# Performance work log

Measured on AMD Instinct MI355X. Metric: run time of the kernel, lower is better.

## Reference

```python
import jax, jax.numpy as jnp
import numpy as np
from jax import lax


def T_grid(t, num_coeff):
    # Chebyshev polynomials T_0..T_{N-1} evaluated at t -> (N, len(t))
    rows = [jnp.ones_like(t), t]
    for _ in range(2, num_coeff):
        rows.append(2.0 * t * rows[-1] - rows[-2])
    return jnp.stack(rows[:num_coeff], axis=0)


def setup_inputs() -> dict:
    key = jax.random.key(0)
    k1, k2, k3, k4, k5 = jax.random.split(key, 5)
    B, D, H, N, T = 128, 512, 1024, 32, 16
    return {
        "t_span": jnp.linspace(0.0, 1.0, T, dtype=jnp.float32),
        "y_init": jax.random.normal(k1, (B, D), dtype=jnp.float32),
        "B_init": jax.random.uniform(k2, (B, D, N), dtype=jnp.float32),
        "W1": jax.random.normal(k3, (D, H), dtype=jnp.float32) / jnp.sqrt(jnp.float32(D)),
        "b1": jax.random.normal(k4, (H,), dtype=jnp.float32),
        "W2": jax.random.normal(k5, (H, D), dtype=jnp.float32) / jnp.sqrt(jnp.float32(H)),
        "num_coeff_per_dim": 32,
        "max_iters": 10,
    }


def reference(t_span, y_init, B_init, W1, b1, W2, num_coeff_per_dim, max_iters):
    N = num_coeff_per_dim
    t0, t1 = t_span[0], t_span[-1]

    # Chebyshev-Gauss-Lobatto nodes on [-1, 1] and Simpson midpoints interleaved
    t_cheb = -jnp.cos(jnp.pi * (jnp.arange(N, dtype=t_span.dtype) / (N - 1)))  # (N,)
    mids = 0.5 * (t_cheb[1:] + t_cheb[:-1])
    t_simpsons = jnp.zeros(2 * N - 1, dtype=t_span.dtype).at[::2].set(t_cheb).at[1::2].set(mids)
    t_true = t0 + 0.5 * (t1 - t0) * (t_simpsons + 1.0)  # (2N-1,)

    Phi_f = T_grid(t_simpsons, N)        # (N, 2N-1)
    Phi = Phi_f[:, ::2]                  # (N, N), invert ONCE (reused every iter)
    Phi_inv = jnp.linalg.inv(Phi)
    widths = (t_true[2::2] - t_true[:-2:2]) / 6.0  # (N-1,) Simpson interval weights

    def f_all(Y):  # vector field f(t, y) = tanh(y @ W1 + t*b1) @ W2, all nodes at once
        # Y: (B, D, M) with M = 2N-1
        h = jnp.tanh(jnp.einsum("bdm,dh->bhm", Y, W1) + t_true[None, None, :] * b1[None, :, None])
        return jnp.einsum("bhm,hd->bdm", h, W2)

    def step(Bc, _):
        approx = jnp.einsum("bdn,nm->bdm", Bc, Phi_f)          # (B, D, 2N-1)
        fap = f_all(approx)
        # Simpson's rule per Chebyshev interval, then cumulative integral S
        s = widths * (fap[..., :-2:2] + 4.0 * fap[..., 1:-1:2] + fap[..., 2::2])  # (B,D,N-1)
        S = jnp.concatenate([jnp.zeros_like(s[..., :1]), jnp.cumsum(s, axis=-1)], axis=-1)
        # torch.linalg.solve(Phi, S + y0, left=False): Bn @ Phi = S + y0
        Bn = (S + y_init[..., None]) @ Phi_inv
        return Bn, None

    B_final, _ = lax.scan(step, B_init, None, length=max_iters)

    t_out = -1.0 + 2.0 * (t_span - t0) / (t1 - t0)
    Phi_out = T_grid(t_out, N)                                  # (N, T)
    approx = jnp.einsum("bdn,nt->bdt", B_final, Phi_out)        # (B, D, T)
    return jnp.moveaxis(approx, -1, 0), B_final                 # (T, B, D), (B, D, N)
```

## Files before the change

kernel.cpp:

```cpp
#include <hip/hip_runtime.h>
#include <hip/hip_bf16.h>
#include <math.h>

#define BB 128
#define DD 512
#define HH 1024
#define NB 32
#define MM 63
#define TT 16
#define ITERS 10

#define OFF_U       0
#define OFF_TTRUE   64
#define OFF_PHIOUT  128
#define OFF_PHIF_BF 1024
#define OFF_QT_BF   2048
#define HDRF        4096
#define OFF_PTPA    HDRF
#define OFF_PTP0    (OFF_PTPA + 2097152)
#define OFF_W1P     (OFF_PTP0 + 2097152)
#define OFF_W2P     (OFF_W1P + 262144)
#define OFF_WWP     (OFF_W2P + 262144)
#define OFF_YW1     (OFF_WWP + 524288)

typedef __attribute__((ext_vector_type(8))) short bf16x8;
typedef __attribute__((ext_vector_type(4))) float f32x4;

static __device__ __forceinline__ unsigned short f2bf(float f) {
    unsigned int x = __builtin_bit_cast(unsigned int, f);
    unsigned int r = x + 0x7FFFu + ((x >> 16) & 1u);
    return (unsigned short)(r >> 16);
}

static __device__ __forceinline__ void store4bf(unsigned short* p,
                                                float v0, float v1, float v2, float v3) {
    unsigned int lo = (unsigned int)f2bf(v0) | ((unsigned int)f2bf(v1) << 16);
    unsigned int hi = (unsigned int)f2bf(v2) | ((unsigned int)f2bf(v3) << 16);
    uint2 u; u.x = lo; u.y = hi;
    *(uint2*)p = u;
}

static __device__ __forceinline__ float tanh_fast(float x) {
    float e = exp2f(x * 2.88539008177793f);
    return 1.0f - 2.0f / (e + 1.0f);
}

static __device__ __forceinline__ unsigned short* aS(unsigned short* smA, int r, int c16) {
    return (unsigned short*)((char*)smA + (((r << 10) + (c16 << 4)) ^ ((r & 7) << 4)));
}

__global__ __launch_bounds__(256) void prologue_kernel(
        const float* __restrict__ t_span, const float* __restrict__ W1,
        const float* __restrict__ W2, const float* __restrict__ y_init,
        float* __restrict__ ws) {
    __shared__ __align__(16) char smem[66560];
    const int bid  = blockIdx.x;
    const int t    = threadIdx.x;
    const int lane = t & 63;
    const int w    = t >> 6;
    const int q    = lane >> 4;
    const int l15  = lane & 15;

    if (bid == 0) {
        double* tsim    = (double*)(smem + 0);
        double* ttrue_d = (double*)(smem + 512);
        double* wid     = (double*)(smem + 1024);
        double* phid    = (double*)(smem + 1280);
        double* pinv    = (double*)(smem + 17408);
        double* Rl      = (double*)(smem + 34048);
        double* Qd      = (double*)(smem + 50176);

        const double PI = 3.14159265358979323846;
        const double t0 = (double)t_span[0];
        const double t1 = (double)t_span[TT - 1];

        if (t < MM) {
            double v;
            if ((t & 1) == 0) {
                int j = t >> 1;
                v = -cos(PI * (double)j / (double)(NB - 1));
            } else {
                int i = t >> 1;
                double a = -cos(PI * (double)i / (double)(NB - 1));
                double b = -cos(PI * (double)(i + 1) / (double)(NB - 1));
                v = 0.5 * (a + b);
            }
            tsim[t] = v;
            ttrue_d[t] = t0 + 0.5 * (t1 - t0) * (v + 1.0);
        }
        __syncthreads();
        if (t < 31) wid[t] = (ttrue_d[2 * t + 2] - ttrue_d[2 * t]) / 6.0;
        if (t < MM) ws[OFF_TTRUE + t] = (float)ttrue_d[t];
        if (t == 63) ws[OFF_TTRUE + 63] = 0.0f;

        if (t < MM) {
            double x = tsim[t];
            double r0 = 1.0, r1 = x;
            phid[0 * MM + t] = r0;
            phid[1 * MM + t] = r1;
            for (int n = 2; n < NB; n++) {
                double r2 = 2.0 * x * r1 - r0;
                phid[n * MM + t] = r2;
                r0 = r1; r1 = r2;
            }
        }

        for (int f = t; f < NB * NB; f += 256) {
            int i = f >> 5, j = f & 31;
            double ci = (i == 0 || i == NB - 1) ? 2.0 : 1.0;
            double cj = (j == 0 || j == NB - 1) ? 2.0 : 1.0;
            double v = 2.0 * cos(PI * (double)(i * j) / (double)(NB - 1))
                       / ((double)(NB - 1) * ci * cj);
            pinv[f] = (j & 1) ? -v : v;
        }
        __syncthreads();

        {
            unsigned short* pf = (unsigned short*)(ws + OFF_PHIF_BF);
            for (int f = t; f < 64 * 32; f += 256) {
                int m = f >> 5, n = f & 31;
                pf[f] = f2bf(m < MM ? (float)phid[n * MM + m] : 0.0f);
            }
        }

        if (t < MM) {
            double acc = 0.0;
            Rl[t * NB + 0] = 0.0;
            for (int i = 1; i < NB; i++) {
                int ip = i - 1;
                double wv = 0.0;
                if (t == 2 * ip)     wv += wid[ip];
                if (t == 2 * ip + 1) wv += 4.0 * wid[ip];
                if (t == 2 * ip + 2) wv += wid[ip];
                acc += wv;
                Rl[t * NB + i] = acc;
            }
        }
        __syncthreads();

        for (int f = t; f < MM * NB; f += 256) {
            int m = f >> 5, j = f & 31;
            double s = 0.0;
            for (int i = 0; i < NB; i++) s += Rl[m * NB + i] * pinv[i * 32 + j];
            Qd[f] = s;
        }
        __syncthreads();

        {
            unsigned short* qt = (unsigned short*)(ws + OFF_QT_BF);
            for (int f = t; f < 32 * 64; f += 256) {
                int j = f >> 6, m = f & 63;
                qt[f] = f2bf(m < MM ? (float)Qd[m * NB + j] : 0.0f);
            }
        }
        if (t < NB) {
            double s = 0.0;
            for (int i = 0; i < NB; i++) s += pinv[i * 32 + t];
            ws[OFF_U + t] = (float)s;
        }
        if (t < TT) {
            double x = -1.0 + 2.0 * ((double)t_span[t] - t0) / (t1 - t0);
            double r0 = 1.0, r1 = x;
            ws[OFF_PHIOUT + 0 * TT + t] = 1.0f;
            ws[OFF_PHIOUT + 1 * TT + t] = (float)x;
            for (int n = 2; n < NB; n++) {
                double r2 = 2.0 * x * r1 - r0;
                ws[OFF_PHIOUT + n * TT + t] = (float)r2;
                r0 = r1; r1 = r2;
            }
        }
        return;
    }

    if (bid <= 64) {
        unsigned short* W1p = (unsigned short*)(ws + OFF_W1P);
        const int hb = bid - 1;
        #pragma unroll
        for (int i = 0; i < 4; i++) {
            int f = i * 256 + t;
            int ds = f >> 6, ln = f & 63;
            int qq = ln >> 4, ll = ln & 15;
            unsigned short tmp[8];
            #pragma unroll
            for (int e = 0; e < 8; e++)
                tmp[e] = f2bf(W1[(size_t)(ds * 32 + qq * 8 + e) * HH + hb * 16 + ll]);
            *(uint4*)(W1p + ((size_t)(hb * 16 + ds) * 64 + ln) * 8) = *(uint4*)tmp;
        }
        return;
    }

    if (bid <= 96) {
        unsigned short* W2p = (unsigned short*)(ws + OFF_W2P);
        const int db = bid - 65;
        #pragma unroll
        for (int i = 0; i < 8; i++) {
            int f = i * 256 + t;
            int hs = f >> 6, ln = f & 63;
            int qq = ln >> 4, ll = ln & 15;
            unsigned short tmp[8];
            #pragma unroll
            for (int e = 0; e < 8; e++)
                tmp[e] = f2bf(W2[(size_t)(hs * 32 + qq * 8 + e) * DD + db * 16 + ll]);
            *(uint4*)(W2p + ((size_t)(db * 32 + hs) * 64 + ln) * 8) = *(uint4*)tmp;
        }
        return;
    }

    unsigned short* lw1t = (unsigned short*)smem;

    if (bid <= 352) {
        unsigned short* WWp = (unsigned short*)(ws + OFF_WWP);
        unsigned short* pbounce = (unsigned short*)(smem + 33280);
        const int idx   = bid - 97;
        const int h2grp = idx & 31;
        const int hpb   = (idx >> 5) * 4 + w;
        const int h2c0  = h2grp * 32;

        for (int i = 0; i < 64; i++) {
            int f = i * 256 + t;
            int row = f >> 5, col = f & 31;
            lw1t[col * 520 + row] = f2bf(W1[(size_t)row * HH + h2c0 + col]);
        }
        __syncthreads();

        f32x4 acc[2][2] = {};
        #pragma unroll 4
        for (int ds = 0; ds < 16; ds++) {
            bf16x8 a[2];
            #pragma unroll
            for (int mt = 0; mt < 2; mt++) {
                const float* w2r = W2 + (size_t)(hpb * 32 + mt * 16 + l15) * DD + ds * 32 + q * 8;
                float4 va = *(const float4*)w2r;
                float4 vb = *(const float4*)(w2r + 4);
                unsigned short tmp[8] = { f2bf(va.x), f2bf(va.y), f2bf(va.z), f2bf(va.w),
                                          f2bf(vb.x), f2bf(vb.y), f2bf(vb.z), f2bf(vb.w) };
                a[mt] = *(bf16x8*)tmp;
            }
            bf16x8 bb0 = *(const bf16x8*)(lw1t + l15 * 520 + ds * 32 + q * 8);
            bf16x8 bb1 = *(const bf16x8*)(lw1t + (16 + l15) * 520 + ds * 32 + q * 8);
            acc[0][0] = __builtin_amdgcn_mfma_f32_16x16x32_bf16(a[0], bb0, acc[0][0], 0, 0, 0);
            acc[0][1] = __builtin_amdgcn_mfma_f32_16x16x32_bf16(a[0], bb1, acc[0][1], 0, 0, 0);
            acc[1][0] = __builtin_amdgcn_mfma_f32_16x16x32_bf16(a[1], bb0, acc[1][0], 0, 0, 0);
            acc[1][1] = __builtin_amdgcn_mfma_f32_16x16x32_bf16(a[1], bb1, acc[1][1], 0, 0, 0);
        }
        unsigned short* pb = pbounce + w * 1024;
        #pragma unroll
        for (int mt = 0; mt < 2; mt++)
            #pragma unroll
            for (int nt = 0; nt < 2; nt++) {
                int lane8 = (mt * 2 + (q >> 1)) * 16 + l15;
                #pragma unroll
                for (int r = 0; r < 4; r++)
                    pb[(nt * 64 + lane8) * 8 + (q & 1) * 4 + r] = f2bf(acc[mt][nt][r]);
            }
        uint4 f0 = *(uint4*)(pb + (0 * 64 + lane) * 8);
        uint4 f1 = *(uint4*)(pb + (1 * 64 + lane) * 8);
        int h2b0 = h2grp * 2;
        *(uint4*)(WWp + ((size_t)(h2b0 + 0) * 32 + hpb) * 512 + lane * 8) = f0;
        *(uint4*)(WWp + ((size_t)(h2b0 + 1) * 32 + hpb) * 512 + lane * 8) = f1;
        return;
    }

    {
        float* yW1 = ws + OFF_YW1;
        const int h2grp = bid - 353;
        const int h2c0  = h2grp * 32;

        for (int i = 0; i < 64; i++) {
            int f = i * 256 + t;
            int row = f >> 5, col = f & 31;
            lw1t[col * 520 + row] = f2bf(W1[(size_t)row * HH + h2c0 + col]);
        }
        __syncthreads();

        f32x4 acc[2][2] = {};
        #pragma unroll 4
        for (int ds = 0; ds < 16; ds++) {
            bf16x8 a[2];
            #pragma unroll
            for (int mt = 0; mt < 2; mt++) {
                const float* yr = y_init + (size_t)(w * 32 + mt * 16 + l15) * DD + ds * 32 + q * 8;
                float4 va = *(const float4*)yr;
                float4 vb = *(const float4*)(yr + 4);
                unsigned short tmp[8] = { f2bf(va.x), f2bf(va.y), f2bf(va.z), f2bf(va.w),
                                          f2bf(vb.x), f2bf(vb.y), f2bf(vb.z), f2bf(vb.w) };
                a[mt] = *(bf16x8*)tmp;
            }
            bf16x8 bb0 = *(const bf16x8*)(lw1t + l15 * 520 + ds * 32 + q * 8);
            bf16x8 bb1 = *(const bf16x8*)(lw1t + (16 + l15) * 520 + ds * 32 + q * 8);
            acc[0][0] = __builtin_amdgcn_mfma_f32_16x16x32_bf16(a[0], bb0, acc[0][0], 0, 0, 0);
            acc[0][1] = __builtin_amdgcn_mfma_f32_16x16x32_bf16(a[0], bb1, acc[0][1], 0, 0, 0);
            acc[1][0] = __builtin_amdgcn_mfma_f32_16x16x32_bf16(a[1], bb0, acc[1][0], 0, 0, 0);
            acc[1][1] = __builtin_amdgcn_mfma_f32_16x16x32_bf16(a[1], bb1, acc[1][1], 0, 0, 0);
        }
        #pragma unroll
        for (int mt = 0; mt < 2; mt++)
            #pragma unroll
            for (int nt = 0; nt < 2; nt++)
                #pragma unroll
                for (int r = 0; r < 4; r++) {
                    int b  = w * 32 + mt * 16 + q * 4 + r;
                    int h2 = h2c0 + nt * 16 + l15;
                    yW1[(size_t)b * HH + h2] = acc[mt][nt][r];
                }
    }
}

__global__ __launch_bounds__(256) void k1_kernel(
        const float* __restrict__ B_init,
        const unsigned short* __restrict__ W1p,
        const float* __restrict__ b1,
        const float* __restrict__ ws,
        unsigned short* __restrict__ Ptp)
{
    __shared__ __align__(16) char smem[40960];
    unsigned short* smA  = (unsigned short*)smem;
    unsigned short* t_sb = (unsigned short*)smem;
    unsigned short* g_sb = (unsigned short*)(smem + 32768);

    const int t    = threadIdx.x;
    const int lane = t & 63;
    const int w    = t >> 6;
    const int q    = lane >> 4;
    const int l15  = lane & 15;
    const int bid  = blockIdx.x;
    const int b    = bid & 127;
    const int hblk = bid >> 7;
    const int hw   = hblk * 128 + w * 32;

    {
        const float* Bi = B_init + (size_t)b * DD * NB;
        #pragma unroll 8
        for (int i = 0; i < 64; i++) {
            int f = i * 256 + t;
            int d = f >> 5, n = f & 31;
            *(unsigned short*)(smem + (((n << 10) + (d << 1)) ^ ((n & 7) << 4)))
                = f2bf(Bi[f]);
        }
    }
    __syncthreads();

    f32x4 acc[2][2] = {};
    const unsigned short* W1b = W1p + (size_t)(hw >> 4) * 8192;
    #pragma unroll 4
    for (int d0 = 0; d0 < DD; d0 += 32) {
        int c16 = (d0 >> 3) + q;
        int ds  = d0 >> 5;
        bf16x8 a0  = *(const bf16x8*)aS(smA, l15, c16);
        bf16x8 a1  = *(const bf16x8*)aS(smA, 16 + l15, c16);
        bf16x8 bb0 = *(const bf16x8*)(W1b + ds * 512 + lane * 8);
        bf16x8 bb1 = *(const bf16x8*)(W1b + 8192 + ds * 512 + lane * 8);
        acc[0][0] = __builtin_amdgcn_mfma_f32_16x16x32_bf16(a0, bb0, acc[0][0], 0, 0, 0);
        acc[0][1] = __builtin_amdgcn_mfma_f32_16x16x32_bf16(a0, bb1, acc[0][1], 0, 0, 0);
        acc[1][0] = __builtin_amdgcn_mfma_f32_16x16x32_bf16(a1, bb0, acc[1][0], 0, 0, 0);
        acc[1][1] = __builtin_amdgcn_mfma_f32_16x16x32_bf16(a1, bb1, acc[1][1], 0, 0, 0);
    }
    #pragma unroll
    for (int mt = 0; mt < 2; mt++)
        #pragma unroll
        for (int nt = 0; nt < 2; nt++) {
            int hl = w * 32 + nt * 16 + l15;
            store4bf(&g_sb[hl * 32 + mt * 16 + q * 4],
                     acc[mt][nt][0], acc[mt][nt][1], acc[mt][nt][2], acc[mt][nt][3]);
        }
    __syncthreads();

    f32x4 zacc[4][2] = {};
    const unsigned short* PF = (const unsigned short*)(ws + OFF_PHIF_BF);
    bf16x8 gb[2];
    #pragma unroll
    for (int nt = 0; nt < 2; nt++)
        gb[nt] = *(const bf16x8*)(&g_sb[(w * 32 + nt * 16 + l15) * 32 + q * 8]);
    #pragma unroll
    for (int mt = 0; mt < 4; mt++) {
        bf16x8 af = *(const bf16x8*)(PF + (mt * 16 + l15) * 32 + q * 8);
        zacc[mt][0] = __builtin_amdgcn_mfma_f32_16x16x32_bf16(af, gb[0], zacc[mt][0], 0, 0, 0);
        zacc[mt][1] = __builtin_amdgcn_mfma_f32_16x16x32_bf16(af, gb[1], zacc[mt][1], 0, 0, 0);
    }

    const float* TTp = ws + OFF_TTRUE;
    float b1v[2] = { b1[hw + l15], b1[hw + 16 + l15] };
    #pragma unroll
    for (int mt = 0; mt < 4; mt++) {
        float4 ttv = *(const float4*)(TTp + mt * 16 + q * 4);
        #pragma unroll
        for (int nt = 0; nt < 2; nt++) {
            int hl = w * 32 + nt * 16 + l15;
            float v0 = tanh_fast(zacc[mt][nt][0] + ttv.x * b1v[nt]);
            float v1 = tanh_fast(zacc[mt][nt][1] + ttv.y * b1v[nt]);
            float v2 = tanh_fast(zacc[mt][nt][2] + ttv.z * b1v[nt]);
            float v3 = tanh_fast(zacc[mt][nt][3] + ttv.w * b1v[nt]);
            store4bf(&t_sb[hl * 72 + mt * 16 + q * 4], v0, v1, v2, v3);
        }
    }
    __syncthreads();

    f32x4 pacc[2][2] = {};
    const unsigned short* QT = (const unsigned short*)(ws + OFF_QT_BF);
    #pragma unroll
    for (int ks = 0; ks < 2; ks++) {
        bf16x8 bt[2];
        #pragma unroll
        for (int nt = 0; nt < 2; nt++)
            bt[nt] = *(const bf16x8*)(&t_sb[(w * 32 + nt * 16 + l15) * 72 + ks * 32 + q * 8]);
        #pragma unroll
        for (int jt = 0; jt < 2; jt++) {
            bf16x8 aq = *(const bf16x8*)(QT + (jt * 16 + l15) * 64 + ks * 32 + q * 8);
            pacc[jt][0] = __builtin_amdgcn_mfma_f32_16x16x32_bf16(aq, bt[0], pacc[jt][0], 0, 0, 0);
            pacc[jt][1] = __builtin_amdgcn_mfma_f32_16x16x32_bf16(aq, bt[1], pacc[jt][1], 0, 0, 0);
        }
    }

    {
        unsigned short* pb = g_sb + w * 1024;
        #pragma unroll
        for (int jt = 0; jt < 2; jt++)
            #pragma unroll
            for (int nt = 0; nt < 2; nt++) {
                int grp = (nt * 2 + (l15 >> 3)) & 3;
                #pragma unroll
                for (int r = 0; r < 4; r++) {
                    int lane8 = grp * 16 + q * 4 + r;
                    pb[(jt * 64 + lane8) * 8 + (l15 & 7)] = f2bf(pacc[jt][nt][r]);
                }
            }
        int hs = hblk * 4 + w;
        uint4 f0 = *(uint4*)(pb + (0 * 64 + lane) * 8);
        uint4 f1 = *(uint4*)(pb + (1 * 64 + lane) * 8);
        *(uint4*)(Ptp + (((size_t)(b * 32 + hs) * 2 + 0) * 64 + lane) * 8) = f0;
        *(uint4*)(Ptp + (((size_t)(b * 32 + hs) * 2 + 1) * 64 + lane) * 8) = f1;
    }
}

__global__ __launch_bounds__(256) void kf_kernel(
        const unsigned short* __restrict__ Ptin,
        const unsigned short* __restrict__ WWp,
        const float* __restrict__ yW1,
        const float* __restrict__ b1,
        const float* __restrict__ ws,
        unsigned short* __restrict__ Ptout)
{
    __shared__ __align__(16) char smem[32768];
    const int t    = threadIdx.x;
    const int lane = t & 63;
    const int w    = t >> 6;
    const int q    = lane >> 4;
    const int l15  = lane & 15;
    const int bid  = blockIdx.x;
    const int b    = bid & 127;
    const int hblk = bid >> 7;
    const int hw   = hblk * 128 + w * 32;

    f32x4 acc[2][2] = {};
    const unsigned short* Ab  = Ptin + (size_t)b * 32768;
    const unsigned short* WWb = WWp + (size_t)(hw >> 4) * 16384;
    unsigned short* buf0 = (unsigned short*)smem;
    unsigned short* buf1 = (unsigned short*)(smem + 16384);

    {
        const uint4* src = (const uint4*)Ab;
        uint4* dst = (uint4*)buf0;
        #pragma unroll
        for (int i = 0; i < 4; i++) dst[i * 256 + t] = src[i * 256 + t];
    }
    __syncthreads();

    #pragma unroll 1
    for (int c = 0; c < 4; ++c) {
        if (c < 3) {
            const uint4* src = (const uint4*)(Ab + (c + 1) * 8192);
            uint4* dst = (uint4*)((c & 1) ? buf0 : buf1);
            #pragma unroll
            for (int i = 0; i < 4; i++) dst[i * 256 + t] = src[i * 256 + t];
        }
        const unsigned short* Ac = (c & 1) ? buf1 : buf0;
        #pragma unroll
        for (int sl = 0; sl < 8; ++sl) {
            int s = c * 8 + sl;
            bf16x8 a0  = *(const bf16x8*)(Ac + (sl * 2 + 0) * 512 + lane * 8);
            bf16x8 a1  = *(const bf16x8*)(Ac + (sl * 2 + 1) * 512 + lane * 8);
            bf16x8 bb0 = *(const bf16x8*)(WWb + s * 512 + lane * 8);
            bf16x8 bb1 = *(const bf16x8*)(WWb + 16384 + s * 512 + lane * 8);
            acc[0][0] = __builtin_amdgcn_mfma_f32_16x16x32_bf16(a0, bb0, acc[0][0], 0, 0, 0);
            acc[0][1] = __builtin_amdgcn_mfma_f32_16x16x32_bf16(a0, bb1, acc[0][1], 0, 0, 0);
            acc[1][0] = __builtin_amdgcn_mfma_f32_16x16x32_bf16(a1, bb0, acc[1][0], 0, 0, 0);
            acc[1][1] = __builtin_amdgcn_mfma_f32_16x16x32_bf16(a1, bb1, acc[1][1], 0, 0, 0);
        }
        __syncthreads();
    }
    unsigned short* g_w = (unsigned short*)(smem + w * 2048);
    unsigned short* t_w = (unsigned short*)(smem + 8192 + w * 4608);
    unsigned short* pb_w = g_w;

    const float* U = ws + OFF_U;
    float yw[2] = { yW1[(size_t)b * HH + hw + l15],
                    yW1[(size_t)b * HH + hw + 16 + l15] };
    #pragma unroll
    for (int mt = 0; mt < 2; mt++) {
        float4 uv = *(const float4*)(U + mt * 16 + q * 4);
        #pragma unroll
        for (int nt = 0; nt < 2; nt++) {
            int hl = nt * 16 + l15;
            store4bf(&g_w[hl * 32 + mt * 16 + q * 4],
                     acc[mt][nt][0] + uv.x * yw[nt],
                     acc[mt][nt][1] + uv.y * yw[nt],
                     acc[mt][nt][2] + uv.z * yw[nt],
                     acc[mt][nt][3] + uv.w * yw[nt]);
        }
    }

    f32x4 zacc[4][2] = {};
    const unsigned short* PF = (const unsigned short*)(ws + OFF_PHIF_BF);
    bf16x8 gb[2];
    #pragma unroll
    for (int nt = 0; nt < 2; nt++)
        gb[nt] = *(const bf16x8*)(&g_w[(nt * 16 + l15) * 32 + q * 8]);
    #pragma unroll
    for (int mt = 0; mt < 4; mt++) {
        bf16x8 af = *(const bf16x8*)(PF + (mt * 16 + l15) * 32 + q * 8);
        zacc[mt][0] = __builtin_amdgcn_mfma_f32_16x16x32_bf16(af, gb[0], zacc[mt][0], 0, 0, 0);
        zacc[mt][1] = __builtin_amdgcn_mfma_f32_16x16x32_bf16(af, gb[1], zacc[mt][1], 0, 0, 0);
    }

    const float* TTp = ws + OFF_TTRUE;
    float b1v[2] = { b1[hw + l15], b1[hw + 16 + l15] };
    #pragma unroll
    for (int mt = 0; mt < 4; mt++) {
        float4 ttv = *(const float4*)(TTp + mt * 16 + q * 4);
        #pragma unroll
        for (int nt = 0; nt < 2; nt++) {
            int hl = nt * 16 + l15;
            float v0 = tanh_fast(zacc[mt][nt][0] + ttv.x * b1v[nt]);
            float v1 = tanh_fast(zacc[mt][nt][1] + ttv.y * b1v[nt]);
            float v2 = tanh_fast(zacc[mt][nt][2] + ttv.z * b1v[nt]);
            float v3 = tanh_fast(zacc[mt][nt][3] + ttv.w * b1v[nt]);
            store4bf(&t_w[hl * 72 + mt * 16 + q * 4], v0, v1, v2, v3);
        }
    }

    f32x4 pacc[2][2] = {};
    const unsigned short* QT = (const unsigned short*)(ws + OFF_QT_BF);
    #pragma unroll
    for (int ks = 0; ks < 2; ks++) {
        bf16x8 bt[2];
        #pragma unroll
        for (int nt = 0; nt < 2; nt++)
            bt[nt] = *(const bf16x8*)(&t_w[(nt * 16 + l15) * 72 + ks * 32 + q * 8]);
        #pragma unroll
        for (int jt = 0; jt < 2; jt++) {
            bf16x8 aq = *(const bf16x8*)(QT + (jt * 16 + l15) * 64 + ks * 32 + q * 8);
            pacc[jt][0] = __builtin_amdgcn_mfma_f32_16x16x32_bf16(aq, bt[0], pacc[jt][0], 0, 0, 0);
            pacc[jt][1] = __builtin_amdgcn_mfma_f32_16x16x32_bf16(aq, bt[1], pacc[jt][1], 0, 0, 0);
        }
    }

    {
        #pragma unroll
        for (int jt = 0; jt < 2; jt++)
            #pragma unroll
            for (int nt = 0; nt < 2; nt++) {
                int grp = (nt * 2 + (l15 >> 3)) & 3;
                #pragma unroll
                for (int r = 0; r < 4; r++) {
                    int lane8 = grp * 16 + q * 4 + r;
                    pb_w[(jt * 64 + lane8) * 8 + (l15 & 7)] = f2bf(pacc[jt][nt][r]);
                }
            }
        int hs = hblk * 4 + w;
        uint4 f0 = *(uint4*)(pb_w + (0 * 64 + lane) * 8);
        uint4 f1 = *(uint4*)(pb_w + (1 * 64 + lane) * 8);
        *(uint4*)(Ptout + (((size_t)(b * 32 + hs) * 2 + 0) * 64 + lane) * 8) = f0;
        *(uint4*)(Ptout + (((size_t)(b * 32 + hs) * 2 + 1) * 64 + lane) * 8) = f1;
    }
}

__global__ __launch_bounds__(256) void k2f_kernel(
        const unsigned short* __restrict__ Ptp,
        const unsigned short* __restrict__ W2p,
        const float* __restrict__ y_init,
        const float* __restrict__ ws,
        float* __restrict__ out)
{
    __shared__ __align__(16) float ls[4 * 544];
    __shared__ float phiout_s[NB * TT];

    const int t    = threadIdx.x;
    const int lane = t & 63;
    const int w    = t >> 6;
    const int q    = lane >> 4;
    const int l15  = lane & 15;
    const int bid  = blockIdx.x;
    const int b    = bid & 127;
    const int dblk = bid >> 7;
    const int dw   = dblk * 64 + w * 16;

    for (int f = t; f < NB * TT; f += 256) phiout_s[f] = ws[OFF_PHIOUT + f];

    f32x4 acc[2] = {};
    const unsigned short* Ab  = Ptp + (size_t)b * 32768;
    const unsigned short* W2b = W2p + (size_t)(dblk * 4 + w) * 16384;
    #pragma unroll 4
    for (int s = 0; s < 32; s++) {
        bf16x8 a0 = *(const bf16x8*)(Ab + (s * 2 + 0) * 512 + lane * 8);
        bf16x8 a1 = *(const bf16x8*)(Ab + (s * 2 + 1) * 512 + lane * 8);
        bf16x8 bb = *(const bf16x8*)(W2b + s * 512 + lane * 8);
        acc[0] = __builtin_amdgcn_mfma_f32_16x16x32_bf16(a0, bb, acc[0], 0, 0, 0);
        acc[1] = __builtin_amdgcn_mfma_f32_16x16x32_bf16(a1, bb, acc[1], 0, 0, 0);
    }

    const float* U = ws + OFF_U;
    float yv = y_init[(size_t)b * DD + dw + l15];
    #pragma unroll
    for (int mt = 0; mt < 2; mt++) {
        float4 uv = *(const float4*)(U + mt * 16 + q * 4);
        #pragma unroll
        for (int r = 0; r < 4; r++) {
            int j = mt * 16 + q * 4 + r;
            float uvr = (r == 0) ? uv.x : (r == 1) ? uv.y : (r == 2) ? uv.z : uv.w;
            ls[w * 544 + j * 17 + l15] = acc[mt][r] + yv * uvr;
        }
    }
    __syncthreads();

    float* out1 = out + (size_t)TT * BB * DD;
    #pragma unroll
    for (int it = 0; it < 8; it++) {
        int f = it * 64 + lane;
        int d_l = f >> 5, j2 = f & 31;
        out1[((size_t)b * DD + dw + d_l) * NB + j2] = ls[w * 544 + j2 * 17 + d_l];
    }

    #pragma unroll
    for (int i = 0; i < 4; i++) {
        int idx = i * 256 + t;
        int t16 = idx >> 6, dl = idx & 63;
        float s = 0.f;
        #pragma unroll
        for (int n = 0; n < NB; n++)
            s += ls[(dl >> 4) * 544 + n * 17 + (dl & 15)] * phiout_s[n * TT + t16];
        out[(size_t)t16 * (BB * DD) + (size_t)b * DD + dblk * 64 + dl] = s;
    }
}

extern "C" void kernel_launch(void* const* d_in, const int* in_sizes, int n_in,
                              void* d_out, int out_size, void* d_ws, size_t ws_size,
                              hipStream_t stream) {
    const float* t_span = (const float*)d_in[0];
    const float* y_init = (const float*)d_in[1];
    const float* B_init = (const float*)d_in[2];
    const float* W1     = (const float*)d_in[3];
    const float* b1     = (const float*)d_in[4];
    const float* W2     = (const float*)d_in[5];
    float* ws  = (float*)d_ws;
    float* out = (float*)d_out;

    unsigned short* W1p  = (unsigned short*)(ws + OFF_W1P);
    unsigned short* W2p  = (unsigned short*)(ws + OFF_W2P);
    unsigned short* WWp  = (unsigned short*)(ws + OFF_WWP);
    float*          yW1  = ws + OFF_YW1;
    unsigned short* PtpA = (unsigned short*)(ws + OFF_PTPA);
    unsigned short* PtpB = (unsigned short*)(ws + OFF_PTP0);

    prologue_kernel<<<dim3(385), 256, 0, stream>>>(t_span, W1, W2, y_init, ws);

    k1_kernel<<<dim3(1024), 256, 0, stream>>>(B_init, W1p, b1, ws, PtpA);

    unsigned short* pin  = PtpA;
    unsigned short* pout = PtpB;
    for (int it = 1; it < ITERS; it++) {
        kf_kernel<<<dim3(1024), 256, 0, stream>>>(pin, WWp, yW1, b1, ws, pout);
        unsigned short* tmp = pin; pin = pout; pout = tmp;
    }
    k2f_kernel<<<dim3(1024), 256, 0, stream>>>(pin, W2p, y_init, ws, out);
}
```

Before: 318.9 us.

## Halve kf_kernel per-block H tile to double grid and occupancy

Each kf_kernel block now covers 64 hidden units instead of 128, with each wave handling 16 columns. The grid doubles to 2048 blocks, shared memory halves to 16KB, and launch_bounds requests 8 blocks per CU, so more waves can stay resident and hide latency. The cost is that each batch row's A operand (Ptin) is streamed from global memory twice as often. The output write is also reorganized so pairs of waves share one staging buffer, which adds an extra block-wide barrier.

Result: slower. 339.4 us (+6.4%).

```diff
diff --git a/kernel.cpp b/kernel.cpp
--- a/kernel.cpp
+++ b/kernel.cpp
@@ -432,7 +432,7 @@
     }
 }
 
-__global__ __launch_bounds__(256) void kf_kernel(
+__global__ __launch_bounds__(256, 8) void kf_kernel(
         const unsigned short* __restrict__ Ptin,
         const unsigned short* __restrict__ WWp,
         const float* __restrict__ yW1,
@@ -440,7 +440,7 @@
         const float* __restrict__ ws,
         unsigned short* __restrict__ Ptout)
 {
-    __shared__ __align__(16) char smem[32768];
+    __shared__ __align__(16) char smem[16384];
     const int t    = threadIdx.x;
     const int lane = t & 63;
     const int w    = t >> 6;
@@ -448,129 +448,110 @@
     const int l15  = lane & 15;
     const int bid  = blockIdx.x;
     const int b    = bid & 127;
-    const int hblk = bid >> 7;
-    const int hw   = hblk * 128 + w * 32;
-
-    f32x4 acc[2][2] = {};
+    const int hb4  = bid >> 7;
+    const int hwv  = hb4 * 64 + w * 16;
+
+    f32x4 acc[2] = {};
     const unsigned short* Ab  = Ptin + (size_t)b * 32768;
-    const unsigned short* WWb = WWp + (size_t)(hw >> 4) * 16384;
+    const unsigned short* WWb = WWp + (size_t)(hb4 * 4 + w) * 16384;
     unsigned short* buf0 = (unsigned short*)smem;
-    unsigned short* buf1 = (unsigned short*)(smem + 16384);
+    unsigned short* buf1 = (unsigned short*)(smem + 8192);
 
     {
         const uint4* src = (const uint4*)Ab;
         uint4* dst = (uint4*)buf0;
-        #pragma unroll
-        for (int i = 0; i < 4; i++) dst[i * 256 + t] = src[i * 256 + t];
+        dst[t] = src[t];
+        dst[256 + t] = src[256 + t];
     }
     __syncthreads();
 
     #pragma unroll 1
-    for (int c = 0; c < 4; ++c) {
-        if (c < 3) {
-            const uint4* src = (const uint4*)(Ab + (c + 1) * 8192);
+    for (int c = 0; c < 8; ++c) {
+        if (c < 7) {
+            const uint4* src = (const uint4*)(Ab + (c + 1) * 4096);
             uint4* dst = (uint4*)((c & 1) ? buf0 : buf1);
-            #pragma unroll
-            for (int i = 0; i < 4; i++) dst[i * 256 + t] = src[i * 256 + t];
+            dst[t] = src[t];
+            dst[256 + t] = src[256 + t];
         }
         const unsigned short* Ac = (c & 1) ? buf1 : buf0;
         #pragma unroll
-        for (int sl = 0; sl < 8; ++sl) {
-            int s = c * 8 + sl;
-            bf16x8 a0  = *(const bf16x8*)(Ac + (sl * 2 + 0) * 512 + lane * 8);
-            bf16x8 a1  = *(const bf16x8*)(Ac + (sl * 2 + 1) * 512 + lane * 8);
-            bf16x8 bb0 = *(const bf16x8*)(WWb + s * 512 + lane * 8);
-            bf16x8 bb1 = *(const bf16x8*)(WWb + 16384 + s * 512 + lane * 8);
-            acc[0][0] = __builtin_amdgcn_mfma_f32_16x16x32_bf16(a0, bb0, acc[0][0], 0, 0, 0);
-            acc[0][1] = __builtin_amdgcn_mfma_f32_16x16x32_bf16(a0, bb1, acc[0][1], 0, 0, 0);
-            acc[1][0] = __builtin_amdgcn_mfma_f32_16x16x32_bf16(a1, bb0, acc[1][0], 0, 0, 0);
-            acc[1][1] = __builtin_amdgcn_mfma_f32_16x16x32_bf16(a1, bb1, acc[1][1], 0, 0, 0);
-        }
-        __syncthreads();
-    }
-    unsigned short* g_w = (unsigned short*)(smem + w * 2048);
-    unsigned short* t_w = (unsigned short*)(smem + 8192 + w * 4608);
-    unsigned short* pb_w = g_w;
+        for (int sl = 0; sl < 4; ++sl) {
+            int s = c * 4 + sl;
+            bf16x8 a0 = *(const bf16x8*)(Ac + (sl * 2 + 0) * 512 + lane * 8);
+            bf16x8 a1 = *(const bf16x8*)(Ac + (sl * 2 + 1) * 512 + lane * 8);
+            bf16x8 bb = *(const bf16x8*)(WWb + s * 512 + lane * 8);
+            acc[0] = __builtin_amdgcn_mfma_f32_16x16x32_bf16(a0, bb, acc[0], 0, 0, 0);
+            acc[1] = __builtin_amdgcn_mfma_f32_16x16x32_bf16(a1, bb, acc[1], 0, 0, 0);
+        }
+        __syncthreads();
+    }
+    unsigned short* g_w = (unsigned short*)(smem + w * 1024);
+    unsigned short* t_w = (unsigned short*)(smem + 4096 + w * 2304);
 
     const float* U = ws + OFF_U;
-    float yw[2] = { yW1[(size_t)b * HH + hw + l15],
-                    yW1[(size_t)b * HH + hw + 16 + l15] };
+    float yw1v = yW1[(size_t)b * HH + hwv + l15];
     #pragma unroll
     for (int mt = 0; mt < 2; mt++) {
         float4 uv = *(const float4*)(U + mt * 16 + q * 4);
-        #pragma unroll
-        for (int nt = 0; nt < 2; nt++) {
-            int hl = nt * 16 + l15;
-            store4bf(&g_w[hl * 32 + mt * 16 + q * 4],
-                     acc[mt][nt][0] + uv.x * yw[nt],
-                     acc[mt][nt][1] + uv.y * yw[nt],
-                     acc[mt][nt][2] + uv.z * yw[nt],
-                     acc[mt][nt][3] + uv.w * yw[nt]);
-        }
-    }
-
-    f32x4 zacc[4][2] = {};
+        store4bf(&g_w[l15 * 32 + mt * 16 + q * 4],
+                 acc[mt][0] + uv.x * yw1v,
+                 acc[mt][1] + uv.y * yw1v,
+                 acc[mt][2] + uv.z * yw1v,
+                 acc[mt][3] + uv.w * yw1v);
+    }
+
+    f32x4 zacc[4] = {};
     const unsigned short* PF = (const unsigned short*)(ws + OFF_PHIF_BF);
-    bf16x8 gb[2];
-    #pragma unroll
-    for (int nt = 0; nt < 2; nt++)
-        gb[nt] = *(const bf16x8*)(&g_w[(nt * 16 + l15) * 32 + q * 8]);
+    bf16x8 gb = *(const bf16x8*)(&g_w[l15 * 32 + q * 8]);
     #pragma unroll
     for (int mt = 0; mt < 4; mt++) {
         bf16x8 af = *(const bf16x8*)(PF + (mt * 16 + l15) * 32 + q * 8);
-        zacc[mt][0] = __builtin_amdgcn_mfma_f32_16x16x32_bf16(af, gb[0], zacc[mt][0], 0, 0, 0);
-        zacc[mt][1] = __builtin_amdgcn_mfma_f32_16x16x32_bf16(af, gb[1], zacc[mt][1], 0, 0, 0);
+        zacc[mt] = __builtin_amdgcn_mfma_f32_16x16x32_bf16(af, gb, zacc[mt], 0, 0, 0);
     }
 
     const float* TTp = ws + OFF_TTRUE;
-    float b1v[2] = { b1[hw + l15], b1[hw + 16 + l15] };
+    float b1v = b1[hwv + l15];
     #pragma unroll
     for (int mt = 0; mt < 4; mt++) {
         float4 ttv = *(const float4*)(TTp + mt * 16 + q * 4);
-        #pragma unroll
-        for (int nt = 0; nt < 2; nt++) {
-            int hl = nt * 16 + l15;
-            float v0 = tanh_fast(zacc[mt][nt][0] + ttv.x * b1v[nt]);
-            float v1 = tanh_fast(zacc[mt][nt][1] + ttv.y * b1v[nt]);
-            float v2 = tanh_fast(zacc[mt][nt][2] + ttv.z * b1v[nt]);
-            float v3 = tanh_fast(zacc[mt][nt][3] + ttv.w * b1v[nt]);
-            store4bf(&t_w[hl * 72 + mt * 16 + q * 4], v0, v1, v2, v3);
-        }
-    }
-
-    f32x4 pacc[2][2] = {};
+        float v0 = tanh_fast(zacc[mt][0] + ttv.x * b1v);
+        float v1 = tanh_fast(zacc[mt][1] + ttv.y * b1v);
+        float v2 = tanh_fast(zacc[mt][2] + ttv.z * b1v);
+        float v3 = tanh_fast(zacc[mt][3] + ttv.w * b1v);
+        store4bf(&t_w[l15 * 72 + mt * 16 + q * 4], v0, v1, v2, v3);
+    }
+
+    f32x4 pacc[2] = {};
     const unsigned short* QT = (const unsigned short*)(ws + OFF_QT_BF);
     #pragma unroll
     for (int ks = 0; ks < 2; ks++) {
-        bf16x8 bt[2];
-        #pragma unroll
-        for (int nt = 0; nt < 2; nt++)
-            bt[nt] = *(const bf16x8*)(&t_w[(nt * 16 + l15) * 72 + ks * 32 + q * 8]);
+        bf16x8 bt = *(const bf16x8*)(&t_w[l15 * 72 + ks * 32 + q * 8]);
         #pragma unroll
         for (int jt = 0; jt < 2; jt++) {
             bf16x8 aq = *(const bf16x8*)(QT + (jt * 16 + l15) * 64 + ks * 32 + q * 8);
-            pacc[jt][0] = __builtin_amdgcn_mfma_f32_16x16x32_bf16(aq, bt[0], pacc[jt][0], 0, 0, 0);
-            pacc[jt][1] = __builtin_amdgcn_mfma_f32_16x16x32_bf16(aq, bt[1], pacc[jt][1], 0, 0, 0);
-        }
-    }
-
+            pacc[jt] = __builtin_amdgcn_mfma_f32_16x16x32_bf16(aq, bt, pacc[jt], 0, 0, 0);
+        }
+    }
+
+    __syncthreads();
     {
-        #pragma unroll
-        for (int jt = 0; jt < 2; jt++)
-            #pragma unroll
-            for (int nt = 0; nt < 2; nt++) {
-                int grp = (nt * 2 + (l15 >> 3)) & 3;
-                #pragma unroll
-                for (int r = 0; r < 4; r++) {
-                    int lane8 = grp * 16 + q * 4 + r;
-                    pb_w[(jt * 64 + lane8) * 8 + (l15 & 7)] = f2bf(pacc[jt][nt][r]);
-                }
-            }
-        int hs = hblk * 4 + w;
-        uint4 f0 = *(uint4*)(pb_w + (0 * 64 + lane) * 8);
-        uint4 f1 = *(uint4*)(pb_w + (1 * 64 + lane) * 8);
-        *(uint4*)(Ptout + (((size_t)(b * 32 + hs) * 2 + 0) * 64 + lane) * 8) = f0;
-        *(uint4*)(Ptout + (((size_t)(b * 32 + hs) * 2 + 1) * 64 + lane) * 8) = f1;
+        unsigned short* pbb = (unsigned short*)smem;
+        const int hs_loc = w >> 1, wp = w & 1;
+        unsigned short* pb_hs = pbb + hs_loc * 1024;
+        #pragma unroll
+        for (int jt = 0; jt < 2; jt++) {
+            int grp = wp * 2 + (l15 >> 3);
+            #pragma unroll
+            for (int r = 0; r < 4; r++) {
+                int lane8 = grp * 16 + q * 4 + r;
+                pb_hs[jt * 512 + lane8 * 8 + (l15 & 7)] = f2bf(pacc[jt][r]);
+            }
+        }
+        __syncthreads();
+        int i = t >> 6;
+        uint4 fv = *(uint4*)(pbb + i * 512 + lane * 8);
+        int hs = hb4 * 2 + (i >> 1), jt = i & 1;
+        *(uint4*)(Ptout + (((size_t)(b * 32 + hs) * 2 + jt) * 64 + lane) * 8) = fv;
     }
 }
 
@@ -668,7 +649,7 @@
     unsigned short* pin  = PtpA;
     unsigned short* pout = PtpB;
     for (int it = 1; it < ITERS; it++) {
-        kf_kernel<<<dim3(1024), 256, 0, stream>>>(pin, WWp, yW1, b1, ws, pout);
+        kf_kernel<<<dim3(2048), 256, 0, stream>>>(pin, WWp, yW1, b1, ws, pout);
         unsigned short* tmp = pin; pin = pout; pout = tmp;
     }
     k2f_kernel<<<dim3(1024), 256, 0, stream>>>(pin, W2p, y_init, ws, out);
```
